# Kernel tuning notes

Hardware: AMD Instinct MI355X
Metric: run time of the kernel (lower is better)

The kernel has to match this reference:

```python
import jax, jax.numpy as jnp
import numpy as np

NUM_CAPSULE = 128   # must equal steps (seq_len) for the reshape in the original code
DIM_CAPSULE = 64
ROUTINGS = 3
EPS = 1e-7          # K.epsilon()


def pos_emb(x):
    """Sinusoidal position embedding added to x over its last two dims [..., S, D].
    Matches the Keras code: evens use sin(pos/10000^(2k/D)), odds use cos with the
    same frequency (odds-1 == 2k), interleaved via stack+reshape."""
    S, D = x.shape[-2], x.shape[-1]
    pos = jnp.arange(S, dtype=x.dtype)[:, None]                      # [S,1]
    inv_freq = 1.0 / jnp.power(10000.0, (2.0 * jnp.arange(D // 2, dtype=x.dtype)) / D)
    ang = pos * inv_freq[None, :]                                    # [S, D/2]
    pe = jnp.stack([jnp.sin(ang), jnp.cos(ang)], axis=-1).reshape(S, D)
    return x + pe


def squash(s):
    ss = jnp.sum(s * s, axis=-1, keepdims=True)
    scale = ss / (1.0 + ss) / jnp.sqrt(ss + EPS)
    return scale * s


def setup_inputs() -> dict:
    key = jax.random.key(0)
    k1, k2 = jax.random.split(key)
    B, steps, in_dim = 32, 128, 256
    u_vecs = jax.random.normal(k1, (B, steps, in_dim), dtype=jnp.float32)
    mask = jnp.ones((B, steps), dtype=jnp.float32)
    # glorot_uniform for capsule kernel (1, in_dim, dim_capsule)
    lim = float(np.sqrt(6.0 / (in_dim + DIM_CAPSULE)))
    W = jax.random.uniform(k2, (1, in_dim, DIM_CAPSULE), jnp.float32, -lim, lim)
    return {"u_vecs": u_vecs, "mask": mask, "W": W}


def reference(u_vecs, mask, W):
    B, steps, in_dim = u_vecs.shape
    N, D = NUM_CAPSULE, DIM_CAPSULE  # N == steps by construction
    # share_weights branch: tile W across steps, permute, add PE, flatten to a conv1d
    # kernel of width 1 -> a plain [in_dim, steps*D] projection matrix.
    tmp = jnp.transpose(jnp.broadcast_to(W, (steps, in_dim, D)), (1, 0, 2))  # [in_dim, steps, D]
    kernel = pos_emb(tmp).reshape(in_dim, steps * D)                          # [in_dim, steps*D]
    u_hat = jnp.einsum('bsi,io->bso', u_vecs, kernel)                         # [B, steps, steps*D]
    u_hat = pos_emb(u_hat)
    u_hat = u_hat.reshape(B, steps, N, D).transpose(0, 2, 1, 3)               # [B, N, In, D]
    b = jnp.zeros((B, N, steps), dtype=u_hat.dtype)                           # routing logits
    m = mask[:, None, :]                                                      # [B, 1, In]
    outputs = None
    for i in range(ROUTINGS):
        # softmax over the num_capsule axis (permute->softmax(-1)->permute in Keras)
        c = jax.nn.softmax(b, axis=1) * m                                     # [B, N, In]
        outputs = squash(jnp.einsum('bni,bnid->bnd', c, u_hat))               # [B, N, D]
        if i < ROUTINGS - 1:
            b = jnp.einsum('bnd,bnid->bni', outputs, u_hat)                   # agreement
    return outputs
```

## Files before the change

kernel.cpp:

```cpp
#include <hip/hip_runtime.h>
#include <math.h>

#define NB 32
#define NS 128
#define NI 256
#define NC 128
#define ND 64

#define L4 9.210340371976184f

__global__ __launch_bounds__(256) void k_prep(const float* __restrict__ u,
                                              const float* __restrict__ W,
                                              float* __restrict__ M,
                                              float* __restrict__ U,
                                              float* __restrict__ PE1) {
    int blk = blockIdx.x;
    int t = threadIdx.x;
    if (blk < 256) {
        __shared__ float us[16][NI];
        __shared__ float ws[128 * ND];
        int r0 = blk * 16;

        {
            const float4* u4 = (const float4*)(u + (size_t)r0 * NI);
            float4* us4 = (float4*)us;
            float up = 0.f;
#pragma unroll
            for (int j = 0; j < 4; ++j) {
                int fi = t * 4 + j;
                float4 v = u4[fi];
                us4[fi] = v;
                up += v.x + v.y + v.z + v.w;
            }
#pragma unroll
            for (int o = 1; o <= 8; o <<= 1) up += __shfl_xor(up, o);
            if ((t & 15) == 0) U[r0 + (t >> 4)] = up;
        }

        int lane = t & 63, w = t >> 6;
        int dp = lane & 31;
        int rh = lane >> 5;
        int rA = w * 4 + rh * 2, rB = rA + 1;
        float2 accA = make_float2(0.f, 0.f), accB = make_float2(0.f, 0.f);
        const float4* W4 = (const float4*)W;

        for (int p = 0; p < 2; ++p) {
            __syncthreads();
            {
                float4* ws4 = (float4*)ws;
#pragma unroll
                for (int j = 0; j < 8; ++j) {
                    int fi = t + 256 * j;
                    ws4[fi] = W4[p * 2048 + fi];
                }
            }
            __syncthreads();
            int ibase = p * 128;
#pragma unroll 8
            for (int ii = 0; ii < 128; ++ii) {
                float2 wv = *(const float2*)&ws[ii * ND + dp * 2];
                float ua = us[rA][ibase + ii];
                float ub = us[rB][ibase + ii];
                accA.x = fmaf(ua, wv.x, accA.x);
                accA.y = fmaf(ua, wv.y, accA.y);
                accB.x = fmaf(ub, wv.x, accB.x);
                accB.y = fmaf(ub, wv.y, accB.y);
            }
        }
        float2* M2 = (float2*)M;
        M2[(size_t)(r0 + rA) * 32 + dp] = accA;
        M2[(size_t)(r0 + rB) * 32 + dp] = accB;
    } else {
        int idx = (blk - 256) * 256 + t;
        int n = idx >> 6, d = idx & 63;
        float ang = (float)n * __expf(-L4 * (float)(d >> 1) * (1.f / 32.f));
        float sv, cv;
        __sincosf(ang, &sv, &cv);
        PE1[idx] = (d & 1) ? cv : sv;
    }
}

__global__ __launch_bounds__(256) void kRed(const float* __restrict__ bl,
                                            const float* __restrict__ mask,
                                            float* __restrict__ mx,
                                            float* __restrict__ minv) {
    int blk = blockIdx.x;
    int b = blk >> 2, s0 = (blk & 3) * 32;
    int t = threadIdx.x;
    int si = t & 31, nh = t >> 5;

    __shared__ float mxp[8][33];
    __shared__ float totp[8][33];

    float v[16];
    float m = -1e30f;
    const float* base = bl + (size_t)(b * NC + nh * 16) * NS + s0 + si;
#pragma unroll
    for (int j = 0; j < 16; ++j) {
        v[j] = base[j * NS];
        m = fmaxf(m, v[j]);
    }
    mxp[nh][si] = m;
    __syncthreads();

    float gm = mxp[0][si];
#pragma unroll
    for (int k = 1; k < 8; ++k) gm = fmaxf(gm, mxp[k][si]);
    float sm = 0.f;
#pragma unroll
    for (int j = 0; j < 16; ++j) sm += __expf(v[j] - gm);
    totp[nh][si] = sm;
    __syncthreads();

    if (t < 32) {
        float tot = 0.f;
#pragma unroll
        for (int k = 0; k < 8; ++k) tot += totp[k][t];
        mx[b * NS + s0 + t] = gm;
        minv[b * NS + s0 + t] = mask[b * NS + s0 + t] / tot;
    }
}

__global__ __launch_bounds__(256, 4) void kR(const float* __restrict__ M,
                                             const float* __restrict__ U,
                                             const float* __restrict__ PE1,
                                             const float* __restrict__ mxg,
                                             const float* __restrict__ minvg,
                                             const float* __restrict__ mask,
                                             float* __restrict__ og,
                                             float* __restrict__ bl,
                                             int first, int last) {
    int bp = blockIdx.x;
    int n  = bp & 127;
    int b0 = (bp >> 7) * 2;
    int t  = threadIdx.x;

    __shared__ float  cs[NS][2];
    __shared__ float  Us[NS][2];
    __shared__ float4 redw[2][4][16];
    __shared__ float4 outs4[2][16];
    __shared__ float  tpar[2][2];
    __shared__ float  sc2[2][2];
    __shared__ float  red2[2][NS * 17];

    {
        int bh = t >> 7, s = t & 127;
        int b = b0 + bh;
        float uu = U[b * NS + s];
        float cv;
        if (first) {
            cv = mask[b * NS + s] * (1.f / 128.f);
        } else {
            cv = __expf(bl[(size_t)(b * NC + n) * NS + s] - mxg[b * NS + s])
                 * minvg[b * NS + s];
        }
        cs[s][bh] = cv;
        Us[s][bh] = uu;
        float p = cv * uu;
#pragma unroll
        for (int o = 32; o > 0; o >>= 1) p += __shfl_xor(p, o);
        if ((t & 63) == 0) tpar[bh][(t >> 6) & 1] = p;
    }

    float4 p14;
    if (t < 32) p14 = ((const float4*)PE1)[n * 16 + (t & 15)];

    int dq = t & 15, sq = t >> 4;
    int s0 = sq * 8;
    int k2 = n * 32 + dq * 2;
    float g0 = __expf(-L4 * (float)k2 * (1.f / 4096.f));
    float g1 = __expf(-L4 * (float)(k2 + 1) * (1.f / 4096.f));
    float sa = __sinf((float)s0 * g0), ca = __cosf((float)s0 * g0);
    float sb = __sinf((float)s0 * g1), cb = __cosf((float)s0 * g1);
    float sg0 = __sinf(g0), cg0 = __cosf(g0);
    float sg1 = __sinf(g1), cg1 = __cosf(g1);
    __syncthreads();

    float4 cc4[4];
    {
        const float4* csp = (const float4*)&cs[s0][0];
        cc4[0] = csp[0]; cc4[1] = csp[1]; cc4[2] = csp[2]; cc4[3] = csp[3];
    }

    const float4* M4a = (const float4*)(M + (size_t)(b0 * NS) * ND) + dq;
    const float4* M4b = M4a + NS * 16;
    float4 va[8], vb[8];
    float4 acc0 = make_float4(0.f, 0.f, 0.f, 0.f);
    float4 acc1 = make_float4(0.f, 0.f, 0.f, 0.f);
#pragma unroll
    for (int i = 0; i < 8; ++i) {
        int s = s0 + i;
        float4 m0 = M4a[s * 16];
        float4 m1 = M4b[s * 16];
        float2 cc = ((const float2*)cc4)[i];
        float4 u0, u1;
        u0.x = m0.x + sa; u0.y = m0.y + ca; u0.z = m0.z + sb; u0.w = m0.w + cb;
        u1.x = m1.x + sa; u1.y = m1.y + ca; u1.z = m1.z + sb; u1.w = m1.w + cb;
        va[i] = u0; vb[i] = u1;
        acc0.x = fmaf(cc.x, u0.x, acc0.x);
        acc0.y = fmaf(cc.x, u0.y, acc0.y);
        acc0.z = fmaf(cc.x, u0.z, acc0.z);
        acc0.w = fmaf(cc.x, u0.w, acc0.w);
        acc1.x = fmaf(cc.y, u1.x, acc1.x);
        acc1.y = fmaf(cc.y, u1.y, acc1.y);
        acc1.z = fmaf(cc.y, u1.z, acc1.z);
        acc1.w = fmaf(cc.y, u1.w, acc1.w);
        float nsa = fmaf(sa, cg0, ca * sg0);
        float nca = fmaf(ca, cg0, -sa * sg0);
        sa = nsa; ca = nca;
        float nsb = fmaf(sb, cg1, cb * sg1);
        float ncb = fmaf(cb, cg1, -sb * sg1);
        sb = nsb; cb = ncb;
    }
#pragma unroll
    for (int o = 16; o <= 32; o <<= 1) {
        acc0.x += __shfl_xor(acc0.x, o); acc0.y += __shfl_xor(acc0.y, o);
        acc0.z += __shfl_xor(acc0.z, o); acc0.w += __shfl_xor(acc0.w, o);
        acc1.x += __shfl_xor(acc1.x, o); acc1.y += __shfl_xor(acc1.y, o);
        acc1.z += __shfl_xor(acc1.z, o); acc1.w += __shfl_xor(acc1.w, o);
    }
    if ((t & 48) == 0) {
        int w = t >> 6;
        redw[0][w][dq] = acc0;
        redw[1][w][dq] = acc1;
    }
    __syncthreads();

    if (t < 32) {
        int bh = t >> 4, q = t & 15;
        float4 r0 = redw[bh][0][q], r1 = redw[bh][1][q];
        float4 r2 = redw[bh][2][q], r3 = redw[bh][3][q];
        float4 o;
        o.x = r0.x + r1.x + r2.x + r3.x;
        o.y = r0.y + r1.y + r2.y + r3.y;
        o.z = r0.z + r1.z + r2.z + r3.z;
        o.w = r0.w + r1.w + r2.w + r3.w;
        float T2 = tpar[bh][0] + tpar[bh][1];
        o.x = fmaf(p14.x, T2, o.x);
        o.y = fmaf(p14.y, T2, o.y);
        o.z = fmaf(p14.z, T2, o.z);
        o.w = fmaf(p14.w, T2, o.w);
        outs4[bh][q] = o;
        float ssq = o.x * o.x + o.y * o.y + o.z * o.z + o.w * o.w;
        float ppu = o.x * p14.x + o.y * p14.y + o.z * p14.z + o.w * p14.w;
#pragma unroll
        for (int o2 = 1; o2 <= 8; o2 <<= 1) {
            ssq += __shfl_xor(ssq, o2);
            ppu += __shfl_xor(ppu, o2);
        }
        if (q == 0) {
            sc2[bh][0] = ssq / (1.f + ssq) * rsqrtf(ssq + 1e-7f);
            sc2[bh][1] = ppu;
        }
    }
    __syncthreads();

    if (last) {
        if (t < 32) {
            int bh = t >> 4, q = t & 15;
            float sc = sc2[bh][0];
            float4 o = outs4[bh][q];
            o.x *= sc; o.y *= sc; o.z *= sc; o.w *= sc;
            ((float4*)og)[((b0 + bh) * NC + n) * 16 + q] = o;
        }
        return;
    }

    float4 oa = outs4[0][dq], ob = outs4[1][dq];
#pragma unroll
    for (int i = 0; i < 8; ++i) {
        int s = s0 + i;
        float4 v0 = va[i], v1 = vb[i];
        red2[0][s * 17 + dq] = v0.x * oa.x + v0.y * oa.y + v0.z * oa.z + v0.w * oa.w;
        red2[1][s * 17 + dq] = v1.x * ob.x + v1.y * ob.y + v1.z * ob.z + v1.w * ob.w;
    }
    __syncthreads();
    {
        int bh = t >> 7, s = t & 127;
        const float* r = &red2[bh][s * 17];
        float sum = 0.f;
#pragma unroll
        for (int q = 0; q < 16; ++q) sum += r[q];
        bl[((b0 + bh) * NC + n) * NS + s] =
            sc2[bh][0] * (sum + sc2[bh][1] * Us[s][bh]);
    }
}

extern "C" void kernel_launch(void* const* d_in, const int* in_sizes, int n_in,
                              void* d_out, int out_size, void* d_ws, size_t ws_size,
                              hipStream_t stream) {
    const float* u    = (const float*)d_in[0];
    const float* mask = (const float*)d_in[1];
    const float* W    = (const float*)d_in[2];
    float* out = (float*)d_out;

    float* ws   = (float*)d_ws;
    float* M    = ws;
    float* U    = M + NB * NS * ND;
    float* PE1  = U + NB * NS;
    float* bl   = PE1 + NC * ND;
    float* mx   = bl + NB * NC * NS;
    float* minv = mx + NB * NS;

    k_prep<<<288, 256, 0, stream>>>(u, W, M, U, PE1);

    kR<<<2048, 256, 0, stream>>>(M, U, PE1, mx, minv, mask, out, bl, 1, 0);
    kRed<<<128, 256, 0, stream>>>(bl, mask, mx, minv);
    kR<<<2048, 256, 0, stream>>>(M, U, PE1, mx, minv, mask, out, bl, 0, 0);
    kRed<<<128, 256, 0, stream>>>(bl, mask, mx, minv);
    kR<<<2048, 256, 0, stream>>>(M, U, PE1, mx, minv, mask, out, bl, 0, 1);
}
```

Before: 98.58 us.

## Process two capsules per block to reuse loaded M rows across capsules

```diff
diff --git a/kernel.cpp b/kernel.cpp
--- a/kernel.cpp
+++ b/kernel.cpp
@@ -121,7 +121,7 @@
     }
 }
 
-__global__ __launch_bounds__(256, 4) void kR(const float* __restrict__ M,
+__global__ __launch_bounds__(256, 3) void kR(const float* __restrict__ M,
                                              const float* __restrict__ U,
                                              const float* __restrict__ PE1,
                                              const float* __restrict__ mxg,
@@ -131,116 +131,143 @@
                                              float* __restrict__ bl,
                                              int first, int last) {
     int bp = blockIdx.x;
-    int n  = bp & 127;
-    int b0 = (bp >> 7) * 2;
+    int n0 = (bp & 63) * 2;
+    int b0 = (bp >> 6) * 2;
     int t  = threadIdx.x;
 
-    __shared__ float  cs[NS][2];
+    __shared__ float4 cs4[NS];
     __shared__ float  Us[NS][2];
-    __shared__ float4 redw[2][4][16];
-    __shared__ float4 outs4[2][16];
-    __shared__ float  tpar[2][2];
-    __shared__ float  sc2[2][2];
-    __shared__ float  red2[2][NS * 17];
+    __shared__ float4 redw[2][2][4][16];
+    __shared__ float4 outs4[2][2][16];
+    __shared__ float  tpar[2][2][2];
+    __shared__ float  sc2[2][2][2];
+    __shared__ float  red2[2][2][NS * 17];
 
     {
         int bh = t >> 7, s = t & 127;
         int b = b0 + bh;
         float uu = U[b * NS + s];
-        float cv;
+        float cv0, cv1;
         if (first) {
-            cv = mask[b * NS + s] * (1.f / 128.f);
+            float mv = mask[b * NS + s] * (1.f / 128.f);
+            cv0 = mv; cv1 = mv;
         } else {
-            cv = __expf(bl[(size_t)(b * NC + n) * NS + s] - mxg[b * NS + s])
-                 * minvg[b * NS + s];
-        }
-        cs[s][bh] = cv;
+            float mxv = mxg[b * NS + s], miv = minvg[b * NS + s];
+            cv0 = __expf(bl[(size_t)(b * NC + n0) * NS + s] - mxv) * miv;
+            cv1 = __expf(bl[(size_t)(b * NC + n0 + 1) * NS + s] - mxv) * miv;
+        }
+        ((float*)&cs4[s])[bh]     = cv0;
+        ((float*)&cs4[s])[2 + bh] = cv1;
         Us[s][bh] = uu;
-        float p = cv * uu;
-#pragma unroll
-        for (int o = 32; o > 0; o >>= 1) p += __shfl_xor(p, o);
-        if ((t & 63) == 0) tpar[bh][(t >> 6) & 1] = p;
+        float p0 = cv0 * uu, p1 = cv1 * uu;
+#pragma unroll
+        for (int o = 32; o > 0; o >>= 1) {
+            p0 += __shfl_xor(p0, o);
+            p1 += __shfl_xor(p1, o);
+        }
+        if ((t & 63) == 0) {
+            tpar[bh][0][(t >> 6) & 1] = p0;
+            tpar[bh][1][(t >> 6) & 1] = p1;
+        }
     }
 
     float4 p14;
-    if (t < 32) p14 = ((const float4*)PE1)[n * 16 + (t & 15)];
+    if (t < 64) {
+        int nh = (t >> 4) & 1, q = t & 15;
+        p14 = ((const float4*)PE1)[(n0 + nh) * 16 + q];
+    }
 
     int dq = t & 15, sq = t >> 4;
     int s0 = sq * 8;
-    int k2 = n * 32 + dq * 2;
-    float g0 = __expf(-L4 * (float)k2 * (1.f / 4096.f));
-    float g1 = __expf(-L4 * (float)(k2 + 1) * (1.f / 4096.f));
-    float sa = __sinf((float)s0 * g0), ca = __cosf((float)s0 * g0);
-    float sb = __sinf((float)s0 * g1), cb = __cosf((float)s0 * g1);
-    float sg0 = __sinf(g0), cg0 = __cosf(g0);
-    float sg1 = __sinf(g1), cg1 = __cosf(g1);
-    __syncthreads();
-
-    float4 cc4[4];
-    {
-        const float4* csp = (const float4*)&cs[s0][0];
-        cc4[0] = csp[0]; cc4[1] = csp[1]; cc4[2] = csp[2]; cc4[3] = csp[3];
-    }
+    int k2 = n0 * 32 + dq * 2;
+    float g00 = __expf(-L4 * (float)k2 * (1.f / 4096.f));
+    float g01 = __expf(-L4 * (float)(k2 + 1) * (1.f / 4096.f));
+    float g10 = __expf(-L4 * (float)(k2 + 32) * (1.f / 4096.f));
+    float g11 = __expf(-L4 * (float)(k2 + 33) * (1.f / 4096.f));
+    float sA0, cA0, sB0, cB0, sA1, cA1, sB1, cB1;
+    __sincosf((float)s0 * g00, &sA0, &cA0);
+    __sincosf((float)s0 * g01, &sB0, &cB0);
+    __sincosf((float)s0 * g10, &sA1, &cA1);
+    __sincosf((float)s0 * g11, &sB1, &cB1);
+    float sg00, cg00, sg01, cg01, sg10, cg10, sg11, cg11;
+    __sincosf(g00, &sg00, &cg00);
+    __sincosf(g01, &sg01, &cg01);
+    __sincosf(g10, &sg10, &cg10);
+    __sincosf(g11, &sg11, &cg11);
+    __syncthreads();
 
     const float4* M4a = (const float4*)(M + (size_t)(b0 * NS) * ND) + dq;
     const float4* M4b = M4a + NS * 16;
     float4 va[8], vb[8];
-    float4 acc0 = make_float4(0.f, 0.f, 0.f, 0.f);
-    float4 acc1 = make_float4(0.f, 0.f, 0.f, 0.f);
+    float4 accA0 = make_float4(0.f, 0.f, 0.f, 0.f);
+    float4 accB0 = make_float4(0.f, 0.f, 0.f, 0.f);
+    float4 accA1 = make_float4(0.f, 0.f, 0.f, 0.f);
+    float4 accB1 = make_float4(0.f, 0.f, 0.f, 0.f);
 #pragma unroll
     for (int i = 0; i < 8; ++i) {
         int s = s0 + i;
         float4 m0 = M4a[s * 16];
         float4 m1 = M4b[s * 16];
-        float2 cc = ((const float2*)cc4)[i];
-        float4 u0, u1;
-        u0.x = m0.x + sa; u0.y = m0.y + ca; u0.z = m0.z + sb; u0.w = m0.w + cb;
-        u1.x = m1.x + sa; u1.y = m1.y + ca; u1.z = m1.z + sb; u1.w = m1.w + cb;
-        va[i] = u0; vb[i] = u1;
-        acc0.x = fmaf(cc.x, u0.x, acc0.x);
-        acc0.y = fmaf(cc.x, u0.y, acc0.y);
-        acc0.z = fmaf(cc.x, u0.z, acc0.z);
-        acc0.w = fmaf(cc.x, u0.w, acc0.w);
-        acc1.x = fmaf(cc.y, u1.x, acc1.x);
-        acc1.y = fmaf(cc.y, u1.y, acc1.y);
-        acc1.z = fmaf(cc.y, u1.z, acc1.z);
-        acc1.w = fmaf(cc.y, u1.w, acc1.w);
-        float nsa = fmaf(sa, cg0, ca * sg0);
-        float nca = fmaf(ca, cg0, -sa * sg0);
-        sa = nsa; ca = nca;
-        float nsb = fmaf(sb, cg1, cb * sg1);
-        float ncb = fmaf(cb, cg1, -sb * sg1);
-        sb = nsb; cb = ncb;
+        va[i] = m0; vb[i] = m1;
+        float4 cc = cs4[s];
+        accA0.x = fmaf(cc.x, m0.x + sA0, accA0.x);
+        accA0.y = fmaf(cc.x, m0.y + cA0, accA0.y);
+        accA0.z = fmaf(cc.x, m0.z + sB0, accA0.z);
+        accA0.w = fmaf(cc.x, m0.w + cB0, accA0.w);
+        accB0.x = fmaf(cc.y, m1.x + sA0, accB0.x);
+        accB0.y = fmaf(cc.y, m1.y + cA0, accB0.y);
+        accB0.z = fmaf(cc.y, m1.z + sB0, accB0.z);
+        accB0.w = fmaf(cc.y, m1.w + cB0, accB0.w);
+        accA1.x = fmaf(cc.z, m0.x + sA1, accA1.x);
+        accA1.y = fmaf(cc.z, m0.y + cA1, accA1.y);
+        accA1.z = fmaf(cc.z, m0.z + sB1, accA1.z);
+        accA1.w = fmaf(cc.z, m0.w + cB1, accA1.w);
+        accB1.x = fmaf(cc.w, m1.x + sA1, accB1.x);
+        accB1.y = fmaf(cc.w, m1.y + cA1, accB1.y);
+        accB1.z = fmaf(cc.w, m1.z + sB1, accB1.z);
+        accB1.w = fmaf(cc.w, m1.w + cB1, accB1.w);
+        float ns, nc;
+        ns = fmaf(sA0, cg00, cA0 * sg00); nc = fmaf(cA0, cg00, -sA0 * sg00); sA0 = ns; cA0 = nc;
+        ns = fmaf(sB0, cg01, cB0 * sg01); nc = fmaf(cB0, cg01, -sB0 * sg01); sB0 = ns; cB0 = nc;
+        ns = fmaf(sA1, cg10, cA1 * sg10); nc = fmaf(cA1, cg10, -sA1 * sg10); sA1 = ns; cA1 = nc;
+        ns = fmaf(sB1, cg11, cB1 * sg11); nc = fmaf(cB1, cg11, -sB1 * sg11); sB1 = ns; cB1 = nc;
     }
 #pragma unroll
     for (int o = 16; o <= 32; o <<= 1) {
-        acc0.x += __shfl_xor(acc0.x, o); acc0.y += __shfl_xor(acc0.y, o);
-        acc0.z += __shfl_xor(acc0.z, o); acc0.w += __shfl_xor(acc0.w, o);
-        acc1.x += __shfl_xor(acc1.x, o); acc1.y += __shfl_xor(acc1.y, o);
-        acc1.z += __shfl_xor(acc1.z, o); acc1.w += __shfl_xor(acc1.w, o);
+        accA0.x += __shfl_xor(accA0.x, o); accA0.y += __shfl_xor(accA0.y, o);
+        accA0.z += __shfl_xor(accA0.z, o); accA0.w += __shfl_xor(accA0.w, o);
+        accB0.x += __shfl_xor(accB0.x, o); accB0.y += __shfl_xor(accB0.y, o);
+        accB0.z += __shfl_xor(accB0.z, o); accB0.w += __shfl_xor(accB0.w, o);
+        accA1.x += __shfl_xor(accA1.x, o); accA1.y += __shfl_xor(accA1.y, o);
+        accA1.z += __shfl_xor(accA1.z, o); accA1.w += __shfl_xor(accA1.w, o);
+        accB1.x += __shfl_xor(accB1.x, o); accB1.y += __shfl_xor(accB1.y, o);
+        accB1.z += __shfl_xor(accB1.z, o); accB1.w += __shfl_xor(accB1.w, o);
     }
     if ((t & 48) == 0) {
         int w = t >> 6;
-        redw[0][w][dq] = acc0;
-        redw[1][w][dq] = acc1;
-    }
-    __syncthreads();
-
-    if (t < 32) {
-        int bh = t >> 4, q = t & 15;
-        float4 r0 = redw[bh][0][q], r1 = redw[bh][1][q];
-        float4 r2 = redw[bh][2][q], r3 = redw[bh][3][q];
+        redw[0][0][w][dq] = accA0;
+        redw[1][0][w][dq] = accB0;
+        redw[0][1][w][dq] = accA1;
+        redw[1][1][w][dq] = accB1;
+    }
+    __syncthreads();
+
+    if (t < 64) {
+        int combo = t >> 4, q = t & 15;
+        int bh = combo >> 1, nh = combo & 1;
+        float4 r0 = redw[bh][nh][0][q], r1 = redw[bh][nh][1][q];
+        float4 r2 = redw[bh][nh][2][q], r3 = redw[bh][nh][3][q];
         float4 o;
         o.x = r0.x + r1.x + r2.x + r3.x;
         o.y = r0.y + r1.y + r2.y + r3.y;
         o.z = r0.z + r1.z + r2.z + r3.z;
         o.w = r0.w + r1.w + r2.w + r3.w;
-        float T2 = tpar[bh][0] + tpar[bh][1];
+        float T2 = tpar[bh][nh][0] + tpar[bh][nh][1];
         o.x = fmaf(p14.x, T2, o.x);
         o.y = fmaf(p14.y, T2, o.y);
         o.z = fmaf(p14.z, T2, o.z);
         o.w = fmaf(p14.w, T2, o.w);
-        outs4[bh][q] = o;
+        outs4[bh][nh][q] = o;
         float ssq = o.x * o.x + o.y * o.y + o.z * o.z + o.w * o.w;
         float ppu = o.x * p14.x + o.y * p14.y + o.z * p14.z + o.w * p14.w;
 #pragma unroll
@@ -249,40 +276,61 @@
             ppu += __shfl_xor(ppu, o2);
         }
         if (q == 0) {
-            sc2[bh][0] = ssq / (1.f + ssq) * rsqrtf(ssq + 1e-7f);
-            sc2[bh][1] = ppu;
+            sc2[bh][nh][0] = ssq / (1.f + ssq) * rsqrtf(ssq + 1e-7f);
+            sc2[bh][nh][1] = ppu;
         }
     }
     __syncthreads();
 
     if (last) {
-        if (t < 32) {
-            int bh = t >> 4, q = t & 15;
-            float sc = sc2[bh][0];
-            float4 o = outs4[bh][q];
+        if (t < 64) {
+            int combo = t >> 4, q = t & 15;
+            int bh = combo >> 1, nh = combo & 1;
+            float sc = sc2[bh][nh][0];
+            float4 o = outs4[bh][nh][q];
             o.x *= sc; o.y *= sc; o.z *= sc; o.w *= sc;
-            ((float4*)og)[((b0 + bh) * NC + n) * 16 + q] = o;
+            ((float4*)og)[((b0 + bh) * NC + n0 + nh) * 16 + q] = o;
         }
         return;
     }
 
-    float4 oa = outs4[0][dq], ob = outs4[1][dq];
+    __sincosf((float)s0 * g00, &sA0, &cA0);
+    __sincosf((float)s0 * g01, &sB0, &cB0);
+    __sincosf((float)s0 * g10, &sA1, &cA1);
+    __sincosf((float)s0 * g11, &sB1, &cB1);
+    float4 oA0 = outs4[0][0][dq], oB0 = outs4[1][0][dq];
+    float4 oA1 = outs4[0][1][dq], oB1 = outs4[1][1][dq];
 #pragma unroll
     for (int i = 0; i < 8; ++i) {
         int s = s0 + i;
-        float4 v0 = va[i], v1 = vb[i];
-        red2[0][s * 17 + dq] = v0.x * oa.x + v0.y * oa.y + v0.z * oa.z + v0.w * oa.w;
-        red2[1][s * 17 + dq] = v1.x * ob.x + v1.y * ob.y + v1.z * ob.z + v1.w * ob.w;
+        float4 m0 = va[i], m1 = vb[i];
+        red2[0][0][s * 17 + dq] = (m0.x + sA0) * oA0.x + (m0.y + cA0) * oA0.y
+                                + (m0.z + sB0) * oA0.z + (m0.w + cB0) * oA0.w;
+        red2[1][0][s * 17 + dq] = (m1.x + sA0) * oB0.x + (m1.y + cA0) * oB0.y
+                                + (m1.z + sB0) * oB0.z + (m1.w + cB0) * oB0.w;
+        red2[0][1][s * 17 + dq] = (m0.x + sA1) * oA1.x + (m0.y + cA1) * oA1.y
+                                + (m0.z + sB1) * oA1.z + (m0.w + cB1) * oA1.w;
+        red2[1][1][s * 17 + dq] = (m1.x + sA1) * oB1.x + (m1.y + cA1) * oB1.y
+                                + (m1.z + sB1) * oB1.z + (m1.w + cB1) * oB1.w;
+        float ns, nc;
+        ns = fmaf(sA0, cg00, cA0 * sg00); nc = fmaf(cA0, cg00, -sA0 * sg00); sA0 = ns; cA0 = nc;
+        ns = fmaf(sB0, cg01, cB0 * sg01); nc = fmaf(cB0, cg01, -sB0 * sg01); sB0 = ns; cB0 = nc;
+        ns = fmaf(sA1, cg10, cA1 * sg10); nc = fmaf(cA1, cg10, -sA1 * sg10); sA1 = ns; cA1 = nc;
+        ns = fmaf(sB1, cg11, cB1 * sg11); nc = fmaf(cB1, cg11, -sB1 * sg11); sB1 = ns; cB1 = nc;
     }
     __syncthreads();
     {
         int bh = t >> 7, s = t & 127;
-        const float* r = &red2[bh][s * 17];
-        float sum = 0.f;
-#pragma unroll
-        for (int q = 0; q < 16; ++q) sum += r[q];
-        bl[((b0 + bh) * NC + n) * NS + s] =
-            sc2[bh][0] * (sum + sc2[bh][1] * Us[s][bh]);
+        float uu = Us[s][bh];
+#pragma unroll
+        for (int nh = 0; nh < 2; ++nh) {
+            const float* r = &red2[bh][nh][s * 17];
+            float sum = 0.f;
+#pragma unroll
+            for (int q = 0; q < 16; ++q) sum += r[q];
+            bl[((b0 + bh) * NC + n0 + nh) * NS + s] =
+                sc2[bh][nh][0] * (sum + sc2[bh][nh][1] * uu);
+        }
     }
 }
 
@@ -304,9 +352,9 @@
 
     k_prep<<<288, 256, 0, stream>>>(u, W, M, U, PE1);
 
-    kR<<<2048, 256, 0, stream>>>(M, U, PE1, mx, minv, mask, out, bl, 1, 0);
+    kR<<<1024, 256, 0, stream>>>(M, U, PE1, mx, minv, mask, out, bl, 1, 0);
     kRed<<<128, 256, 0, stream>>>(bl, mask, mx, minv);
-    kR<<<2048, 256, 0, stream>>>(M, U, PE1, mx, minv, mask, out, bl, 0, 0);
+    kR<<<1024, 256, 0, stream>>>(M, U, PE1, mx, minv, mask, out, bl, 0, 0);
     kRed<<<128, 256, 0, stream>>>(bl, mask, mx, minv);
-    kR<<<2048, 256, 0, stream>>>(M, U, PE1, mx, minv, mask, out, bl, 0, 1);
+    kR<<<1024, 256, 0, stream>>>(M, U, PE1, mx, minv, mask, out, bl, 0, 1);
 }
```

After: 126.6 us. +28.4%, slower.
